# Kernel optimization log

Measured on AMD Instinct MI355X. Metric: run time of the kernel, lower is better.

## Reference

```python
import jax, jax.numpy as jnp
import numpy as np

N_LAYERS = 8
DILATIONS = [1, 2, 1, 2, 1, 2, 1, 2]
K_HOPS = 3
BN = 13248   # batch(64) * n_nodes(207), merged as in the torch module
L = 13       # 12 history steps + 1; shrinks by sum(dilations)=12 across layers
E = 211968   # BN * avg_degree(16)


def _conv1d(x, w, b, dil):
    # x: (BN, Cin, L), w: (Cout, Cin, 2) kernel-2 dilated conv, VALID (causal shrink)
    y = jax.lax.conv_general_dilated(x, w, (1,), 'VALID', rhs_dilation=(dil,),
                                     dimension_numbers=('NCH', 'OIH', 'NCH'))
    return y + b[None, :, None]


def setup_inputs() -> dict:
    key = jax.random.key(0)
    ks = jax.random.split(key, 20)
    s = 0.1  # keep activations in a sane range
    return {
        'x': jax.random.normal(ks[0], (BN, L, 2), jnp.float32),
        'edge_src': jax.random.randint(ks[1], (E,), 0, BN),
        'edge_dst': jax.random.randint(ks[2], (E,), 0, BN),
        'edge_w': jax.random.uniform(ks[3], (E,), jnp.float32),
        'init_w': s * jax.random.normal(ks[4], (2, 32), jnp.float32),
        'init_b': s * jax.random.normal(ks[5], (32,), jnp.float32),
        'filt_w': s * jax.random.normal(ks[6], (8, 32, 32, 2), jnp.float32),
        'filt_b': s * jax.random.normal(ks[7], (8, 32), jnp.float32),
        'gate_w': s * jax.random.normal(ks[8], (8, 32, 32, 2), jnp.float32),
        'gate_b': s * jax.random.normal(ks[9], (8, 32), jnp.float32),
        'gcn_w': s * jax.random.normal(ks[10], (8, 6, 32, 32), jnp.float32),
        'gcn_b': s * jax.random.normal(ks[11], (8, 32), jnp.float32),
        'skip_w': s * jax.random.normal(ks[12], (8, 256, 32), jnp.float32),
        'skip_b': s * jax.random.normal(ks[13], (8, 256), jnp.float32),
        'out0_w': s * jax.random.normal(ks[14], (256, 512), jnp.float32),
        'out0_b': s * jax.random.normal(ks[15], (512,), jnp.float32),
        'out1_w': s * jax.random.normal(ks[16], (512, 12), jnp.float32),
        'out1_b': s * jax.random.normal(ks[17], (12,), jnp.float32),
    }


def reference(x, edge_src, edge_dst, edge_w, init_w, init_b,
              filt_w, filt_b, gate_w, gate_b, gcn_w, gcn_b,
              skip_w, skip_b, out0_w, out0_b, out1_w, out1_b):
    # init linear: (BN, L, 2) -> (BN, L, 32) -> (BN, 32, L)
    h = (x @ init_w + init_b).transpose(0, 2, 1)
    # per-hop edge weights: elementwise powers of the transition weights
    # (faithful to repo's dense_to_sparse(transition ** k)); bck = transposed edges
    adjs = [(edge_src, edge_dst, edge_w ** k) for k in range(1, K_HOPS + 1)] + \
           [(edge_dst, edge_src, edge_w ** k) for k in range(1, K_HOPS + 1)]
    skip = None
    for l in range(N_LAYERS):
        d = DILATIONS[l]
        res = h
        # Gated TCN: tanh(filter) * sigmoid(gate), seq shrinks by d
        t = jnp.tanh(_conv1d(h, filt_w[l], filt_b[l], d)) * \
            jax.nn.sigmoid(_conv1d(h, gate_w[l], gate_b[l], d))
        # Diffusion conv: sum over 6 adjacency types of A_w (x W_a)
        xt = t.transpose(0, 2, 1)  # (BN, L', 32)
        g = jnp.zeros_like(xt)
        for a, (src, dst, w) in enumerate(adjs):
            msg = (xt @ gcn_w[l, a])[src] * w[:, None, None]  # (E, L', 32)
            g = g + jax.ops.segment_sum(msg, dst, num_segments=BN)
        h = g.transpose(0, 2, 1) + gcn_b[l][None, :, None]  # (BN, 32, L')
        # residual connection (align shrunk sequence)
        h = h + res[:, :, -h.shape[-1]:]
        # skip conv (1x1) on last timestep, accumulated
        sc = h[:, :, -1] @ skip_w[l].T + skip_b[l]  # (BN, 256)
        skip = sc if skip is None else skip + sc
    out = jax.nn.relu(skip)
    out = jax.nn.relu(out @ out0_w + out0_b)
    return out @ out1_w + out1_b  # (BN, 12)
```

## Files before the change

### kernel.cpp

```cpp
#include <hip/hip_runtime.h>
#include <hip/hip_fp16.h>

#define BN 13248
#define NE 211968
#define NBKT 8
#define SCAN_TOT (BN * NBKT)
#define SCAN_NBLK 52
#define ZSTRIDE 200
#define HSTRIDE 40
#define HNODE 480

typedef __attribute__((ext_vector_type(8))) short bf16x8;
typedef __attribute__((ext_vector_type(8))) _Float16 f16x8;
typedef __attribute__((ext_vector_type(4))) float f32x4;

__device__ __forceinline__ f32x4 mfma16b(bf16x8 a, bf16x8 b, f32x4 c) {
  return __builtin_amdgcn_mfma_f32_16x16x32_bf16(a, b, c, 0, 0, 0);
}
__device__ __forceinline__ f32x4 mfma16h(f16x8 a, f16x8 b, f32x4 c) {
  return __builtin_amdgcn_mfma_f32_16x16x32_f16(a, b, c, 0, 0, 0);
}

__device__ __forceinline__ unsigned short to_bf16(float v) {
  unsigned bits = __float_as_uint(v);
  return (unsigned short)((bits + 0x7FFFu + ((bits >> 16) & 1u)) >> 16);
}
__device__ __forceinline__ unsigned short to_f16(float v) {
  union { __half h; unsigned short s; } u; u.h = __float2half(v); return u.s;
}
__device__ __forceinline__ unsigned h2u(__half2 h) {
  union { __half2 h; unsigned u; } v; v.h = h; return v.u;
}
__device__ __forceinline__ __half2 u2h(unsigned u) {
  union { unsigned u; __half2 h; } v; v.u = u; return v.h;
}

__device__ __forceinline__ float fast_tanh(float x) {
  float e2 = __expf(2.f * x);
  return 1.f - 2.f / (e2 + 1.f);
}
__device__ __forceinline__ float fast_sig(float x) {
  return 1.f / (1.f + __expf(-x));
}

__global__ void k_count(const int* __restrict__ src, const int* __restrict__ dst,
                        int* __restrict__ cur_f, int* __restrict__ cur_b) {
  int e = blockIdx.x * 256 + threadIdx.x;
  if (e < NE) {
    int s = src[e], t = dst[e];
    atomicAdd(&cur_f[t * NBKT + (s >> 11)], 1);
    atomicAdd(&cur_b[s * NBKT + (t >> 11)], 1);
  }
}

__global__ __launch_bounds__(1024) void k_scan1(int* __restrict__ cnt_f, int* __restrict__ cnt_b,
                                                int* __restrict__ bsum) {
  __shared__ int sdata[1024];
  int b = blockIdx.x;
  int dir = (b >= SCAN_NBLK) ? 1 : 0;
  int lb = dir ? b - SCAN_NBLK : b;
  int* cnt = dir ? cnt_b : cnt_f;
  int tid = threadIdx.x;
  int i0 = lb * 2048 + tid * 2;
  int v0 = (i0 < SCAN_TOT) ? cnt[i0] : 0;
  int v1 = (i0 + 1 < SCAN_TOT) ? cnt[i0 + 1] : 0;
  int tot = v0 + v1;
  sdata[tid] = tot;
  __syncthreads();
  for (int off = 1; off < 1024; off <<= 1) {
    int add = (tid >= off) ? sdata[tid - off] : 0;
    __syncthreads();
    sdata[tid] += add;
    __syncthreads();
  }
  int excl = sdata[tid] - tot;
  if (i0 < SCAN_TOT) cnt[i0] = excl;
  if (i0 + 1 < SCAN_TOT) cnt[i0 + 1] = excl + v0;
  if (tid == 1023) bsum[b] = sdata[1023];
}

__global__ void k_scan2(int* __restrict__ bsum) {
  __shared__ int sdata[128];
  int tid = threadIdx.x;
  int seg = (tid >= 64) ? 64 : 0;
  int src = (tid < 64) ? tid : tid - 64 + SCAN_NBLK;
  int valid = ((tid & 63) < SCAN_NBLK);
  int v = valid ? bsum[src] : 0;
  sdata[tid] = v;
  __syncthreads();
  for (int off = 1; off < 64; off <<= 1) {
    int add = (tid - off >= seg) ? sdata[tid - off] : 0;
    __syncthreads();
    sdata[tid] += add;
    __syncthreads();
  }
  if (valid) bsum[src] = sdata[tid] - v;
}

__global__ __launch_bounds__(1024) void k_scan3(int* __restrict__ cnt_f, int* __restrict__ cnt_b,
                                                const int* __restrict__ bsum,
                                                int* __restrict__ row_f, int* __restrict__ row_b) {
  int b = blockIdx.x;
  int dir = (b >= SCAN_NBLK) ? 1 : 0;
  int lb = dir ? b - SCAN_NBLK : b;
  int* cnt = dir ? cnt_b : cnt_f;
  int* row = dir ? row_b : row_f;
  int off = bsum[b];
  int tid = threadIdx.x;
#pragma unroll
  for (int k = 0; k < 2; ++k) {
    int idx = lb * 2048 + tid * 2 + k;
    if (idx < SCAN_TOT) {
      int v = cnt[idx] + off;
      cnt[idx] = v;
      if ((idx & (NBKT - 1)) == 0) row[idx / NBKT] = v;
    }
  }
  if (b == 0 && tid == 0) { row_f[BN] = NE; row_b[BN] = NE; }
}

__global__ void k_fill(const int* __restrict__ src, const int* __restrict__ dst,
                       const float* __restrict__ w,
                       int* __restrict__ cur_f, int4* __restrict__ ce_f,
                       int* __restrict__ cur_b, int4* __restrict__ ce_b) {
  int e = blockIdx.x * 256 + threadIdx.x;
  if (e < NE) {
    int s = src[e], t = dst[e];
    float wv = w[e];
    float w2 = wv * wv, w3 = w2 * wv;
    int u1 = (int)h2u(__float2half2_rn(wv));
    int u2 = (int)h2u(__float2half2_rn(w2));
    int u3 = (int)h2u(__float2half2_rn(w3));
    int p = atomicAdd(&cur_f[t * NBKT + (s >> 11)], 1); ce_f[p] = make_int4(s, u1, u2, u3);
    int q = atomicAdd(&cur_b[s * NBKT + (t >> 11)], 1); ce_b[q] = make_int4(t, u1, u2, u3);
  }
}

__global__ void k_init(const float* __restrict__ x, const float* __restrict__ iw,
                       const float* __restrict__ ib, float* __restrict__ h) {
  int idx = blockIdx.x * 256 + threadIdx.x;
  if (idx >= BN * 13 * 32) return;
  int c = idx & 31;
  int r = idx >> 5;
  int n = r % BN;
  int tau = r / BN;
  float x0 = x[(n * 13 + tau) * 2 + 0];
  float x1 = x[(n * 13 + tau) * 2 + 1];
  h[idx] = fmaf(x0, iw[c], fmaf(x1, iw[32 + c], ib[c]));
}

__global__ void k_pack(const float* __restrict__ skip_w, const float* __restrict__ skip_b,
                       const float* __restrict__ w0, const float* __restrict__ w1,
                       const float* __restrict__ gcn_w,
                       const float* __restrict__ filt_w, const float* __restrict__ gate_w,
                       unsigned short* __restrict__ SWb, unsigned short* __restrict__ W0T,
                       unsigned short* __restrict__ W1T, float* __restrict__ bsum,
                       unsigned short* __restrict__ Gg16, unsigned short* __restrict__ WTC) {
  int id = blockIdx.x * 256 + threadIdx.x;
  if (id < 65536) {
    int j = id >> 8, k = id & 255;
    SWb[id] = to_bf16(skip_w[((k >> 5) * 256 + j) * 32 + (k & 31)]);
  }
  if (id < 131072) {
    int jo = id >> 8, k = id & 255;
    W0T[id] = to_bf16(w0[k * 512 + jo]);
  }
  if (id < 8192) {
    int n = id >> 9, k = id & 511;
    W1T[id] = (n < 12) ? to_bf16(w1[k * 12 + n]) : (unsigned short)0;
  }
  if (id < 256) {
    float s = 0.f;
    for (int l = 0; l < 8; ++l) s += skip_b[l * 256 + id];
    bsum[id] = s;
  }
  if (id < 49152) {
    int l = id / 6144, rem = id % 6144;
    int co = rem / 192, k = rem % 192;
    int a = k >> 5, ci = k & 31;
    Gg16[id] = to_f16(gcn_w[((l * 6 + a) * 32 + ci) * 32 + co]);
  }
  if (id < 32768) {
    int l = id >> 12, rem = id & 4095;
    int g = rem >> 11, co = (rem >> 6) & 31, k = rem & 63;
    const float* srcw = (g ? gate_w : filt_w) + l * 2048;
    float v = (k < 32) ? srcw[(co * 32 + k) * 2 + 0] : srcw[(co * 32 + (k - 32)) * 2 + 1];
    WTC[id] = to_f16(v);
  }
}

template<int LIN, int D, int TPAD>
__global__ __launch_bounds__(256) void k_tcn(const float* __restrict__ h_in, unsigned short* __restrict__ t_out,
    const float* __restrict__ fw, const float* __restrict__ fb,
    const float* __restrict__ gw, const float* __restrict__ gb) {
  constexpr int LOUT = LIN - D;
  __shared__ __align__(16) float wq[32 * 32 * 4];
  __shared__ float hl[8][LIN * 32];
  int tid = threadIdx.x;
  for (int f = tid; f < 4096; f += 256) {
    int e = f & 3, co = (f >> 2) & 31, ci = f >> 7;
    const float* srcw = (e < 2) ? fw : gw;
    wq[f] = srcw[(co * 32 + ci) * 2 + (e & 1)];
  }
  int n0 = blockIdx.x * 8;
  for (int i = tid; i < 8 * LIN * 32; i += 256) {
    int c = i & 31, r = i >> 5;
    int nl = r / LIN, tau = r % LIN;
    hl[nl][tau * 32 + c] = h_in[(tau * BN + n0 + nl) * 32 + c];
  }
  __syncthreads();
  int nl = tid >> 5, co = tid & 31;
  int n = n0 + nl;
  float accf[LOUT], accg[LOUT];
  float fbv = fb[co], gbv = gb[co];
#pragma unroll
  for (int j = 0; j < LOUT; ++j) { accf[j] = fbv; accg[j] = gbv; }
#pragma unroll
  for (int ci = 0; ci < 32; ++ci) {
    float4 wv = *(const float4*)&wq[(ci * 32 + co) * 4];
    float xr[LIN];
#pragma unroll
    for (int t = 0; t < LIN; ++t) xr[t] = hl[nl][t * 32 + ci];
#pragma unroll
    for (int j = 0; j < LOUT; ++j) {
      accf[j] = fmaf(xr[j], wv.x, accf[j]);
      accf[j] = fmaf(xr[j + D], wv.y, accf[j]);
      accg[j] = fmaf(xr[j], wv.z, accg[j]);
      accg[j] = fmaf(xr[j + D], wv.w, accg[j]);
    }
  }
#pragma unroll
  for (int j = 0; j < TPAD; ++j) {
    unsigned short v = 0;
    if (j < LOUT) v = to_f16(fast_tanh(accf[j < LOUT ? j : 0]) * fast_sig(accg[j < LOUT ? j : 0]));
    t_out[(n * TPAD + j) * 32 + co] = v;
  }
}

template<int TPAD, int NT>
__device__ __forceinline__ void edge_fma(const int4& c, const uint2 (&u)[NT], __half2* A) {
  __half2 wh0 = u2h((unsigned)c.y), wh1 = u2h((unsigned)c.z), wh2 = u2h((unsigned)c.w);
#pragma unroll
  for (int j = 0; j < NT; ++j) {
    __half2 v0 = u2h(u[j].x), v1 = u2h(u[j].y);
    A[(0 * NT + j) * 2 + 0] = __hfma2(wh0, v0, A[(0 * NT + j) * 2 + 0]);
    A[(0 * NT + j) * 2 + 1] = __hfma2(wh0, v1, A[(0 * NT + j) * 2 + 1]);
    A[(1 * NT + j) * 2 + 0] = __hfma2(wh1, v0, A[(1 * NT + j) * 2 + 0]);
    A[(1 * NT + j) * 2 + 1] = __hfma2(wh1, v1, A[(1 * NT + j) * 2 + 1]);
    A[(2 * NT + j) * 2 + 0] = __hfma2(wh2, v0, A[(2 * NT + j) * 2 + 0]);
    A[(2 * NT + j) * 2 + 1] = __hfma2(wh2, v1, A[(2 * NT + j) * 2 + 1]);
  }
}

template<int TPAD, int NT, int LOUTT>
__device__ __forceinline__ void gather_dir(const unsigned short* __restrict__ t_in,
    int e0, int e1, const int4* __restrict__ ce, int rowoff0, int rowbase, __half2* A) {
  constexpr bool FULL = (LOUTT >= TPAD);
  constexpr int EB = 4;
  int e = e0;
  for (; e + EB <= e1; e += EB) {
    int4 c[EB];
    uint2 u[EB][NT];
#pragma unroll
    for (int k = 0; k < EB; ++k) c[k] = ce[e + k];
#pragma unroll
    for (int k = 0; k < EB; ++k) {
      const unsigned short* p = t_in + c[k].x * (TPAD * 32) + rowoff0;
#pragma unroll
      for (int j = 0; j < NT; ++j) {
        if (FULL || rowbase + j < LOUTT) u[k][j] = *(const uint2*)(p + j * 32);
        else u[k][j] = make_uint2(0u, 0u);
      }
    }
#pragma unroll
    for (int k = 0; k < EB; ++k) edge_fma<TPAD, NT>(c[k], u[k], A);
  }
  for (; e < e1; ++e) {
    int4 c = ce[e];
    uint2 u[NT];
    const unsigned short* p = t_in + c.x * (TPAD * 32) + rowoff0;
#pragma unroll
    for (int j = 0; j < NT; ++j) {
      if (FULL || rowbase + j < LOUTT) u[j] = *(const uint2*)(p + j * 32);
      else u[j] = make_uint2(0u, 0u);
    }
    edge_fma<TPAD, NT>(c, u, A);
  }
}

template<int LOUT, int D, int TPAD, int D2, int TPAD2, bool LAST>
__global__ __launch_bounds__(128, 4) void k_fused(
    const unsigned short* __restrict__ t_in,
    const float* __restrict__ h_in, float* __restrict__ h_out,
    float* __restrict__ lastcol, unsigned short* __restrict__ t_next,
    const int* __restrict__ row_f, const int4* __restrict__ ce_f,
    const int* __restrict__ row_b, const int4* __restrict__ ce_b,
    const unsigned short* __restrict__ Wg,
    const float* __restrict__ bias,
    const unsigned short* __restrict__ Wtc,
    const float* __restrict__ fbn, const float* __restrict__ gbn) {
  constexpr int NT = TPAD / 4;
  constexpr int LOUT2 = LAST ? 1 : (LOUT - D2);
  constexpr int SBYTES = 4 * TPAD * ZSTRIDE * 2;
  __shared__ __align__(16) char smem[SBYTES];
  unsigned short* Zl = (unsigned short*)smem;
  unsigned short* hb16 = (unsigned short*)smem;
  int tid = threadIdx.x;
  int nl = tid >> 5, lane32 = tid & 31;
  int tl = lane32 >> 3;
  int c4 = (lane32 & 7) << 2;
  int n0 = blockIdx.x * 4;
  int n = n0 + nl;
  int rowbase = tl * NT;
  int rowoff0 = rowbase * 32 + c4;
  int ef0 = row_f[n], ef1 = row_f[n + 1];
  int eb0 = row_b[n], eb1 = row_b[n + 1];
  __half2 acc[6 * NT * 2];
  __half2 zero = __float2half2_rn(0.f);
#pragma unroll
  for (int i = 0; i < 6 * NT * 2; ++i) acc[i] = zero;
  gather_dir<TPAD, NT, LOUT>(t_in, ef0, ef1, ce_f, rowoff0, rowbase, acc);
  gather_dir<TPAD, NT, LOUT>(t_in, eb0, eb1, ce_b, rowoff0, rowbase, acc + 3 * NT * 2);
#pragma unroll
  for (int j = 0; j < NT; ++j) {
    int m = nl * TPAD + rowbase + j;
#pragma unroll
    for (int a = 0; a < 6; ++a) {
      uint2 v = make_uint2(h2u(acc[(a * NT + j) * 2 + 0]), h2u(acc[(a * NT + j) * 2 + 1]));
      *(uint2*)(&Zl[m * ZSTRIDE + a * 32 + c4]) = v;
    }
  }
  __syncthreads();
  int wave = tid >> 6, lane = tid & 63;
  int m16 = lane & 15, q = lane >> 4;
  f32x4 dacc[NT];
#pragma unroll
  for (int i = 0; i < NT; ++i) {
    int u = wave * NT + i;
    int mt = u >> 1, nt = u & 1;
    dacc[i] = (f32x4){0.f, 0.f, 0.f, 0.f};
#pragma unroll
    for (int ks = 0; ks < 6; ++ks) {
      f16x8 av = *(const f16x8*)(&Zl[(mt * 16 + m16) * ZSTRIDE + ks * 32 + q * 8]);
      f16x8 bv = *(const f16x8*)((const _Float16*)Wg + (nt * 16 + m16) * 192 + ks * 32 + q * 8);
      dacc[i] = mfma16h(av, bv, dacc[i]);
    }
  }
  __syncthreads();
#pragma unroll
  for (int i = 0; i < NT; ++i) {
    int u = wave * NT + i;
    int mt = u >> 1, nt = u & 1;
    int co = nt * 16 + m16;
    float bco = bias[co];
#pragma unroll
    for (int r = 0; r < 4; ++r) {
      int mm = mt * 16 + q * 4 + r;
      int node = mm / TPAD;
      int tau = mm % TPAD;
      if (tau < LOUT) {
        float rres = h_in[((tau + D) * BN + n0 + node) * 32 + co];
        float o = dacc[i][r] + bco + rres;
        h_out[(tau * BN + n0 + node) * 32 + co] = o;
        if (!LAST) hb16[node * HNODE + tau * HSTRIDE + co] = to_f16(o);
        if (tau == LOUT - 1) lastcol[(n0 + node) * 32 + co] = o;
      }
    }
  }
  if (!LAST) {
    __syncthreads();
#pragma unroll
    for (int i = 0; i < 4; ++i) {
      int u = wave * 4 + i;
      int node = u >> 1, ntc = u & 1;
      int co = ntc * 16 + m16;
      f32x4 df = (f32x4){0.f, 0.f, 0.f, 0.f};
      f32x4 dg = (f32x4){0.f, 0.f, 0.f, 0.f};
#pragma unroll
      for (int s = 0; s < 2; ++s) {
        f16x8 av = *(const f16x8*)(&hb16[node * HNODE + (m16 + s * D2) * HSTRIDE + q * 8]);
        f16x8 bvf = *(const f16x8*)((const _Float16*)Wtc + (0 * 32 + co) * 64 + s * 32 + q * 8);
        f16x8 bvg = *(const f16x8*)((const _Float16*)Wtc + (1 * 32 + co) * 64 + s * 32 + q * 8);
        df = mfma16h(av, bvf, df);
        dg = mfma16h(av, bvg, dg);
      }
      float fbv = fbn[co], gbv = gbn[co];
#pragma unroll
      for (int r = 0; r < 4; ++r) {
        int j = q * 4 + r;
        if (j < TPAD2) {
          unsigned short v = 0;
          if (j < LOUT2)
            v = to_f16(fast_tanh(df[r] + fbv) * fast_sig(dg[r] + gbv));
          t_next[((n0 + node) * TPAD2 + j) * 32 + co] = v;
        }
      }
    }
  }
}

__device__ __forceinline__ bf16x8 ldsA(const unsigned short* buf, int stride, int row, int ks, int q) {
  int unit = ks * 4 + q;
  int addr = row * stride + ((unit ^ (row & 7)) << 3);
  return *(const bf16x8*)(buf + addr);
}

__global__ __launch_bounds__(256) void k_final(const float* __restrict__ lastcol,
    const unsigned short* __restrict__ SWb, const unsigned short* __restrict__ W0T,
    const unsigned short* __restrict__ W1T, const float* __restrict__ bsum,
    const float* __restrict__ b0, const float* __restrict__ b1,
    float* __restrict__ out) {
  __shared__ __align__(16) unsigned short Z[32 * 256];
  __shared__ __align__(16) unsigned short H[32 * 512];
  int tid = threadIdx.x;
  int wave = tid >> 6, lane = tid & 63;
  int m16 = lane & 15, q = lane >> 4;
  int n0 = blockIdx.x * 32;
#pragma unroll
  for (int it = 0; it < 32; ++it) {
    int id = it * 256 + tid;
    int m = id >> 8, k = id & 255;
    float v = lastcol[((k >> 5) * BN + n0 + m) * 32 + (k & 31)];
    Z[m * 256 + (((k >> 3) ^ (m & 7)) << 3) + (k & 7)] = to_bf16(v);
  }
  __syncthreads();
  f32x4 acc1[2][4];
#pragma unroll
  for (int mt = 0; mt < 2; ++mt)
#pragma unroll
    for (int i = 0; i < 4; ++i) acc1[mt][i] = (f32x4){0.f, 0.f, 0.f, 0.f};
#pragma unroll
  for (int ks = 0; ks < 8; ++ks) {
    bf16x8 a0 = ldsA(Z, 256, m16, ks, q);
    bf16x8 a1 = ldsA(Z, 256, 16 + m16, ks, q);
#pragma unroll
    for (int i = 0; i < 4; ++i) {
      int j = (wave * 4 + i) * 16 + m16;
      bf16x8 b = *(const bf16x8*)(SWb + j * 256 + ks * 32 + q * 8);
      acc1[0][i] = mfma16b(a0, b, acc1[0][i]);
      acc1[1][i] = mfma16b(a1, b, acc1[1][i]);
    }
  }
  __syncthreads();
#pragma unroll
  for (int i = 0; i < 4; ++i) {
    int j = (wave * 4 + i) * 16 + m16;
    float bs = bsum[j];
#pragma unroll
    for (int mt = 0; mt < 2; ++mt)
#pragma unroll
      for (int r = 0; r < 4; ++r) {
        int row = mt * 16 + q * 4 + r;
        float v = fmaxf(acc1[mt][i][r] + bs, 0.f);
        Z[row * 256 + (((j >> 3) ^ (row & 7)) << 3) + (j & 7)] = to_bf16(v);
      }
  }
  __syncthreads();
  f32x4 acc2[2][8];
#pragma unroll
  for (int mt = 0; mt < 2; ++mt)
#pragma unroll
    for (int i = 0; i < 8; ++i) acc2[mt][i] = (f32x4){0.f, 0.f, 0.f, 0.f};
#pragma unroll
  for (int ks = 0; ks < 8; ++ks) {
    bf16x8 a0 = ldsA(Z, 256, m16, ks, q);
    bf16x8 a1 = ldsA(Z, 256, 16 + m16, ks, q);
#pragma unroll
    for (int i = 0; i < 8; ++i) {
      int jo = (wave * 8 + i) * 16 + m16;
      bf16x8 b = *(const bf16x8*)(W0T + jo * 256 + ks * 32 + q * 8);
      acc2[0][i] = mfma16b(a0, b, acc2[0][i]);
      acc2[1][i] = mfma16b(a1, b, acc2[1][i]);
    }
  }
#pragma unroll
  for (int i = 0; i < 8; ++i) {
    int jo = (wave * 8 + i) * 16 + m16;
    float b0v = b0[jo];
#pragma unroll
    for (int mt = 0; mt < 2; ++mt)
#pragma unroll
      for (int r = 0; r < 4; ++r) {
        int row = mt * 16 + q * 4 + r;
        float v = fmaxf(acc2[mt][i][r] + b0v, 0.f);
        H[row * 512 + (((jo >> 3) ^ (row & 7)) << 3) + (jo & 7)] = to_bf16(v);
      }
  }
  __syncthreads();
  if (wave < 2) {
    f32x4 acc3 = (f32x4){0.f, 0.f, 0.f, 0.f};
#pragma unroll
    for (int ks = 0; ks < 16; ++ks) {
      bf16x8 a = ldsA(H, 512, wave * 16 + m16, ks, q);
      bf16x8 b = *(const bf16x8*)(W1T + m16 * 512 + ks * 32 + q * 8);
      acc3 = mfma16b(a, b, acc3);
    }
    if (m16 < 12) {
      float bv = b1[m16];
#pragma unroll
      for (int r = 0; r < 4; ++r)
        out[(n0 + wave * 16 + q * 4 + r) * 12 + m16] = acc3[r] + bv;
    }
  }
}

extern "C" void kernel_launch(void* const* d_in, const int* in_sizes, int n_in,
                              void* d_out, int out_size, void* d_ws, size_t ws_size,
                              hipStream_t stream) {
  const float* x      = (const float*)d_in[0];
  const int*   esrc   = (const int*)d_in[1];
  const int*   edst   = (const int*)d_in[2];
  const float* ew     = (const float*)d_in[3];
  const float* init_w = (const float*)d_in[4];
  const float* init_b = (const float*)d_in[5];
  const float* filt_w = (const float*)d_in[6];
  const float* filt_b = (const float*)d_in[7];
  const float* gate_w = (const float*)d_in[8];
  const float* gate_b = (const float*)d_in[9];
  const float* gcn_w  = (const float*)d_in[10];
  const float* gcn_b  = (const float*)d_in[11];
  const float* skip_w = (const float*)d_in[12];
  const float* skip_b = (const float*)d_in[13];
  const float* w0     = (const float*)d_in[14];
  const float* b0     = (const float*)d_in[15];
  const float* w1     = (const float*)d_in[16];
  const float* b1     = (const float*)d_in[17];
  float* out = (float*)d_out;

  float* base = (float*)d_ws;
  float* hA      = base;
  float* hB      = hA + 13 * BN * 32;
  unsigned short* tA = (unsigned short*)(hB + 13 * BN * 32);
  unsigned short* tB = tA + 12 * BN * 32;
  float* lastcol = (float*)(tB + 12 * BN * 32);
  int* row_f = (int*)(lastcol + 8 * BN * 32);
  int* row_b = row_f + (BN + 2);
  int* bscan = row_b + (BN + 2);
  int* cur_f = bscan + 128;
  int* cur_b = cur_f + BN * NBKT;
  int4* ce_f = (int4*)(cur_b + BN * NBKT);
  int4* ce_b = ce_f + NE;
  unsigned short* SWb  = (unsigned short*)(ce_b + NE);
  unsigned short* W0T  = SWb + 65536;
  unsigned short* W1T  = W0T + 131072;
  unsigned short* Gg16 = W1T + 8192;
  unsigned short* WTC  = Gg16 + 49152;
  float* bsumv = (float*)(WTC + 32768);

  hipMemsetAsync(cur_f, 0, 2 * BN * NBKT * sizeof(int), stream);
  const int egrid = (NE + 255) / 256;
  k_count<<<egrid, 256, 0, stream>>>(esrc, edst, cur_f, cur_b);
  k_scan1<<<2 * SCAN_NBLK, 1024, 0, stream>>>(cur_f, cur_b, bscan);
  k_scan2<<<1, 128, 0, stream>>>(bscan);
  k_scan3<<<2 * SCAN_NBLK, 1024, 0, stream>>>(cur_f, cur_b, bscan, row_f, row_b);
  k_fill<<<egrid, 256, 0, stream>>>(esrc, edst, ew, cur_f, ce_f, cur_b, ce_b);
  k_init<<<(BN * 13 * 32 + 255) / 256, 256, 0, stream>>>(x, init_w, init_b, hA);
  k_pack<<<512, 256, 0, stream>>>(skip_w, skip_b, w0, w1, gcn_w, filt_w, gate_w,
                                  SWb, W0T, W1T, bsumv, Gg16, WTC);

  k_tcn<13, 1, 12><<<BN / 8, 256, 0, stream>>>(hA, tA, filt_w, filt_b, gate_w, gate_b);

#define FUSED(l, LOUTv, Dv, TPv, D2v, TP2v, LASTv, tin, tout, hin, hout) \
  k_fused<LOUTv, Dv, TPv, D2v, TP2v, LASTv><<<BN / 4, 128, 0, stream>>>( \
      tin, hin, hout, lastcol + l * BN * 32, tout, row_f, ce_f, row_b, ce_b, \
      Gg16 + l * 6144, gcn_b + l * 32, WTC + (l + 1) * 4096, \
      filt_b + (l + 1) * 32, gate_b + (l + 1) * 32);

  FUSED(0, 12, 1, 12, 2, 12, false, tA, tB, hA, hB)
  FUSED(1, 10, 2, 12, 1, 12, false, tB, tA, hB, hA)
  FUSED(2,  9, 1, 12, 2,  8, false, tA, tB, hA, hB)
  FUSED(3,  7, 2,  8, 1,  8, false, tB, tA, hB, hA)
  FUSED(4,  6, 1,  8, 2,  4, false, tA, tB, hA, hB)
  FUSED(5,  4, 2,  4, 1,  4, false, tB, tA, hB, hA)
  FUSED(6,  3, 1,  4, 2,  4, false, tA, tB, hA, hB)
#undef FUSED
  k_fused<1, 2, 4, 2, 4, true><<<BN / 4, 128, 0, stream>>>(
      tB, hB, hA, lastcol + 7 * BN * 32, tA, row_f, ce_f, row_b, ce_b,
      Gg16 + 7 * 6144, gcn_b + 7 * 32, WTC, filt_b, gate_b);

  k_final<<<BN / 32, 256, 0, stream>>>(lastcol, SWb, W0T, W1T, bsumv, b0, b1, out);
}
```

Baseline: 620.8 us.

## Interleave time rows in t buffers and gather forward/backward edges together

```diff
diff --git a/kernel.cpp b/kernel.cpp
--- a/kernel.cpp
+++ b/kernel.cpp
@@ -194,6 +194,7 @@
     const float* __restrict__ fw, const float* __restrict__ fb,
     const float* __restrict__ gw, const float* __restrict__ gb) {
   constexpr int LOUT = LIN - D;
+  constexpr int NTC = TPAD / 4;
   __shared__ __align__(16) float wq[32 * 32 * 4];
   __shared__ float hl[8][LIN * 32];
   int tid = threadIdx.x;
@@ -233,7 +234,8 @@
   for (int j = 0; j < TPAD; ++j) {
     unsigned short v = 0;
     if (j < LOUT) v = to_f16(fast_tanh(accf[j < LOUT ? j : 0]) * fast_sig(accg[j < LOUT ? j : 0]));
-    t_out[(n * TPAD + j) * 32 + co] = v;
+    int rp = (j % NTC) * 4 + j / NTC;
+    t_out[(n * TPAD + rp) * 32 + co] = v;
   }
 }
 
@@ -253,9 +255,19 @@
 }
 
 template<int TPAD, int NT, int LOUTT>
+__device__ __forceinline__ void gd_loads(const unsigned short* __restrict__ t_in, const int4& c,
+                                         int base_off, int tlNT, uint2 (&u)[NT]) {
+  const unsigned short* p = t_in + c.x * (TPAD * 32) + base_off;
+#pragma unroll
+  for (int j = 0; j < NT; ++j) {
+    if (LOUTT >= TPAD || tlNT + j < LOUTT) u[j] = *(const uint2*)(p + j * 128);
+    else u[j] = make_uint2(0u, 0u);
+  }
+}
+
+template<int TPAD, int NT, int LOUTT>
 __device__ __forceinline__ void gather_dir(const unsigned short* __restrict__ t_in,
-    int e0, int e1, const int4* __restrict__ ce, int rowoff0, int rowbase, __half2* A) {
-  constexpr bool FULL = (LOUTT >= TPAD);
+    int e0, int e1, const int4* __restrict__ ce, int base_off, int tlNT, __half2* A) {
   constexpr int EB = 4;
   int e = e0;
   for (; e + EB <= e1; e += EB) {
@@ -264,28 +276,42 @@
 #pragma unroll
     for (int k = 0; k < EB; ++k) c[k] = ce[e + k];
 #pragma unroll
-    for (int k = 0; k < EB; ++k) {
-      const unsigned short* p = t_in + c[k].x * (TPAD * 32) + rowoff0;
-#pragma unroll
-      for (int j = 0; j < NT; ++j) {
-        if (FULL || rowbase + j < LOUTT) u[k][j] = *(const uint2*)(p + j * 32);
-        else u[k][j] = make_uint2(0u, 0u);
-      }
-    }
+    for (int k = 0; k < EB; ++k) gd_loads<TPAD, NT, LOUTT>(t_in, c[k], base_off, tlNT, u[k]);
 #pragma unroll
     for (int k = 0; k < EB; ++k) edge_fma<TPAD, NT>(c[k], u[k], A);
   }
   for (; e < e1; ++e) {
     int4 c = ce[e];
     uint2 u[NT];
-    const unsigned short* p = t_in + c.x * (TPAD * 32) + rowoff0;
-#pragma unroll
-    for (int j = 0; j < NT; ++j) {
-      if (FULL || rowbase + j < LOUTT) u[j] = *(const uint2*)(p + j * 32);
-      else u[j] = make_uint2(0u, 0u);
-    }
+    gd_loads<TPAD, NT, LOUTT>(t_in, c, base_off, tlNT, u);
     edge_fma<TPAD, NT>(c, u, A);
   }
+}
+
+template<int TPAD, int NT, int LOUTT>
+__device__ __forceinline__ void gather_both(const unsigned short* __restrict__ t_in,
+    int ef0, int ef1, const int4* __restrict__ cef,
+    int eb0, int eb1, const int4* __restrict__ ceb,
+    int base_off, int tlNT, __half2* Af, __half2* Ab) {
+  constexpr int EB = (NT >= 3) ? 3 : 4;
+  int ef = ef0, eb = eb0;
+  while (ef + EB <= ef1 && eb + EB <= eb1) {
+    int4 cf[EB], cb[EB];
+#pragma unroll
+    for (int k = 0; k < EB; ++k) { cf[k] = cef[ef + k]; cb[k] = ceb[eb + k]; }
+    uint2 uf[EB][NT], ub[EB][NT];
+#pragma unroll
+    for (int k = 0; k < EB; ++k) gd_loads<TPAD, NT, LOUTT>(t_in, cf[k], base_off, tlNT, uf[k]);
+#pragma unroll
+    for (int k = 0; k < EB; ++k) gd_loads<TPAD, NT, LOUTT>(t_in, cb[k], base_off, tlNT, ub[k]);
+#pragma unroll
+    for (int k = 0; k < EB; ++k) edge_fma<TPAD, NT>(cf[k], uf[k], Af);
+#pragma unroll
+    for (int k = 0; k < EB; ++k) edge_fma<TPAD, NT>(cb[k], ub[k], Ab);
+    ef += EB; eb += EB;
+  }
+  gather_dir<TPAD, NT, LOUTT>(t_in, ef, ef1, cef, base_off, tlNT, Af);
+  gather_dir<TPAD, NT, LOUTT>(t_in, eb, eb1, ceb, base_off, tlNT, Ab);
 }
 
 template<int LOUT, int D, int TPAD, int D2, int TPAD2, bool LAST>
@@ -300,6 +326,7 @@
     const unsigned short* __restrict__ Wtc,
     const float* __restrict__ fbn, const float* __restrict__ gbn) {
   constexpr int NT = TPAD / 4;
+  constexpr int NT2 = TPAD2 / 4;
   constexpr int LOUT2 = LAST ? 1 : (LOUT - D2);
   constexpr int SBYTES = 4 * TPAD * ZSTRIDE * 2;
   __shared__ __align__(16) char smem[SBYTES];
@@ -311,23 +338,24 @@
   int c4 = (lane32 & 7) << 2;
   int n0 = blockIdx.x * 4;
   int n = n0 + nl;
-  int rowbase = tl * NT;
-  int rowoff0 = rowbase * 32 + c4;
+  int base_off = tl * 32 + c4;
+  int tlNT = tl * NT;
   int ef0 = row_f[n], ef1 = row_f[n + 1];
   int eb0 = row_b[n], eb1 = row_b[n + 1];
-  __half2 acc[6 * NT * 2];
+  __half2 accf[3 * NT * 2], accb[3 * NT * 2];
   __half2 zero = __float2half2_rn(0.f);
 #pragma unroll
-  for (int i = 0; i < 6 * NT * 2; ++i) acc[i] = zero;
-  gather_dir<TPAD, NT, LOUT>(t_in, ef0, ef1, ce_f, rowoff0, rowbase, acc);
-  gather_dir<TPAD, NT, LOUT>(t_in, eb0, eb1, ce_b, rowoff0, rowbase, acc + 3 * NT * 2);
+  for (int i = 0; i < 3 * NT * 2; ++i) { accf[i] = zero; accb[i] = zero; }
+  gather_both<TPAD, NT, LOUT>(t_in, ef0, ef1, ce_f, eb0, eb1, ce_b, base_off, tlNT, accf, accb);
 #pragma unroll
   for (int j = 0; j < NT; ++j) {
-    int m = nl * TPAD + rowbase + j;
-#pragma unroll
-    for (int a = 0; a < 6; ++a) {
-      uint2 v = make_uint2(h2u(acc[(a * NT + j) * 2 + 0]), h2u(acc[(a * NT + j) * 2 + 1]));
-      *(uint2*)(&Zl[m * ZSTRIDE + a * 32 + c4]) = v;
+    int m = nl * TPAD + tlNT + j;
+#pragma unroll
+    for (int a = 0; a < 3; ++a) {
+      uint2 vf = make_uint2(h2u(accf[(a * NT + j) * 2 + 0]), h2u(accf[(a * NT + j) * 2 + 1]));
+      uint2 vb = make_uint2(h2u(accb[(a * NT + j) * 2 + 0]), h2u(accb[(a * NT + j) * 2 + 1]));
+      *(uint2*)(&Zl[m * ZSTRIDE + a * 32 + c4]) = vf;
+      *(uint2*)(&Zl[m * ZSTRIDE + (a + 3) * 32 + c4]) = vb;
     }
   }
   __syncthreads();
@@ -392,7 +420,8 @@
           unsigned short v = 0;
           if (j < LOUT2)
             v = to_f16(fast_tanh(df[r] + fbv) * fast_sig(dg[r] + gbv));
-          t_next[((n0 + node) * TPAD2 + j) * 32 + co] = v;
+          int rp = (j % NT2) * 4 + j / NT2;
+          t_next[((n0 + node) * TPAD2 + rp) * 32 + co] = v;
         }
       }
     }
```

After: 642.8 us. 1.04x slower.
